# Optimization experiments

Measured on AMD Instinct MI355X. Metric: run time of the kernel, lower is better.

Reference implementation:

```python
import jax
import jax.numpy as jnp
from jax import lax
import numpy as np

DIM = 256
WIN = 7


def setup_inputs() -> dict:
    key = jax.random.key(0)
    ks = jax.random.split(key, 7)
    B, C, H, W = 16, DIM, 64, 64
    k = WIN
    return {
        "x": jax.random.normal(ks[0], (B, C, H, W), dtype=jnp.float32),
        "dw_weight": jax.random.normal(ks[1], (C, 1, k, k), dtype=jnp.float32) * 0.1,
        "pw_weight": jax.random.normal(ks[2], (C, C), dtype=jnp.float32) * 0.05,
        "w1": jax.random.normal(ks[3], (C // 4, C), dtype=jnp.float32) * 0.05,
        "b1": jax.random.normal(ks[4], (C // 4,), dtype=jnp.float32) * 0.05,
        "w2": jax.random.normal(ks[5], (C * k * k, C // 4), dtype=jnp.float32) * 0.05,
        "b2": jax.random.normal(ks[6], (C * k * k,), dtype=jnp.float32) * 0.05,
    }


def reference(x, dw_weight, pw_weight, w1, b1, w2, b2):
    B, C, H, W = x.shape
    k = dw_weight.shape[-1]
    pad = k // 2
    # dynamic kernel generator: global avg pool -> 1x1 conv -> GELU -> 1x1 conv
    pooled = x.mean(axis=(2, 3))                                  # [B, C]
    h = jax.nn.gelu(pooled @ w1.T + b1, approximate=False)        # [B, C//4]
    dyn = (h @ w2.T + b2).reshape(B, C, 1, k, k)                  # [B, C, 1, k, k]
    # fuse static depthwise weights with dynamic per-sample weights
    fused = dw_weight[None] + dyn                                  # [B, C, 1, k, k]
    # per-instance depthwise conv via groups = B*C
    x_flat = x.reshape(1, B * C, H, W)
    kern = fused.reshape(B * C, 1, k, k)
    out = lax.conv_general_dilated(
        x_flat, kern,
        window_strides=(1, 1),
        padding=[(pad, pad), (pad, pad)],
        feature_group_count=B * C,
        dimension_numbers=("NCHW", "OIHW", "NCHW"),
    )
    out = out.reshape(B, C, H, W)
    # final 1x1 pointwise conv (no bias)
    return jnp.einsum("bchw,oc->bohw", out, pw_weight)
```

## Files before the change

kernel.cpp:

```cpp
#include <hip/hip_runtime.h>
#include <math.h>
#include <stdint.h>

typedef __attribute__((ext_vector_type(8))) short short8;
typedef __attribute__((ext_vector_type(4))) float f32x4;

#define B_  16
#define C_  256
#define HW_ 4096
#define KK_ 49
#define CR_ 64

__device__ __forceinline__ ushort f2bf(float f) {
    union { float f; uint32_t u; } v; v.f = f;
    uint32_t r = (v.u + 0x7FFFu + ((v.u >> 16) & 1u)) >> 16;
    return (ushort)r;
}

__global__ __launch_bounds__(256) void pool_kernel(const float* __restrict__ x,
                                                   float* __restrict__ pooled) {
    int bc = blockIdx.x;
    const float4* p4 = (const float4*)(x + (size_t)bc * HW_);
    float s = 0.f;
    for (int i = threadIdx.x; i < HW_ / 4; i += 256) {
        float4 v = p4[i];
        s += (v.x + v.y) + (v.z + v.w);
    }
#pragma unroll
    for (int off = 32; off > 0; off >>= 1) s += __shfl_down(s, off);
    __shared__ float red[4];
    if ((threadIdx.x & 63) == 0) red[threadIdx.x >> 6] = s;
    __syncthreads();
    if (threadIdx.x == 0)
        pooled[bc] = (red[0] + red[1] + red[2] + red[3]) * (1.f / HW_);
}

__global__ __launch_bounds__(64) void mlp_kernel(const float* __restrict__ pooled,
                                                 const float* __restrict__ w1,
                                                 const float* __restrict__ b1,
                                                 float* __restrict__ h) {
    int b = blockIdx.x;
    int r = threadIdx.x;
    __shared__ float pr[C_];
    for (int i = r; i < C_; i += 64) pr[i] = pooled[b * C_ + i];
    __syncthreads();
    float acc = b1[r];
    const float* wr = w1 + (size_t)r * C_;
    for (int c = 0; c < C_; c += 4) {
        float4 wv = *(const float4*)(wr + c);
        acc += pr[c] * wv.x + pr[c + 1] * wv.y + pr[c + 2] * wv.z + pr[c + 3] * wv.w;
    }
    h[b * CR_ + r] = 0.5f * acc * (1.f + erff(acc * 0.70710678118654752f));
}

__global__ __launch_bounds__(256) void genw_kernel(const float* __restrict__ h,
                                                   const float* __restrict__ w2,
                                                   const float* __restrict__ b2,
                                                   const float* __restrict__ dw,
                                                   float* __restrict__ fused) {
    __shared__ float hs[B_ * CR_];
    int m = blockIdx.x * 256 + threadIdx.x;
    for (int i = threadIdx.x; i < B_ * CR_; i += 256) hs[i] = h[i];
    float wrow[CR_];
    const float4* w4 = (const float4*)(w2 + (size_t)m * CR_);
#pragma unroll
    for (int i = 0; i < CR_ / 4; i++) {
        float4 v = w4[i];
        wrow[4 * i] = v.x; wrow[4 * i + 1] = v.y;
        wrow[4 * i + 2] = v.z; wrow[4 * i + 3] = v.w;
    }
    float base = b2[m] + dw[m];
    __syncthreads();
    for (int b = 0; b < B_; b++) {
        float acc = base;
        const float* hb = hs + b * CR_;
#pragma unroll
        for (int r = 0; r < CR_; r++) acc += hb[r] * wrow[r];
        fused[(size_t)b * (C_ * KK_) + m] = acc;
    }
}

__global__ __launch_bounds__(256) void prep_kernel(const float* __restrict__ pw,
                                                   ushort* __restrict__ Pa) {
    int idx = blockIdx.x * 256 + threadIdx.x;
    int o = idx >> 8, c = idx & 255;
    Pa[(size_t)(((o >> 4) * 32) + (c >> 3)) * 128 + (o & 15) * 8 + (c & 7)] = f2bf(pw[idx]);
}

__global__ __launch_bounds__(512, 4) void dw_kernel(const float* __restrict__ x,
                                                    const float* __restrict__ fused,
                                                    ushort* __restrict__ Ug) {
    __shared__ __align__(16) char smem[52352];
    float*  xs  = (float*)smem;
    ushort* Us  = (ushort*)smem;
    float*  wsm = (float*)(smem + 50688);

    const int strip = blockIdx.x;
    const int cb    = blockIdx.y;
    const int b     = blockIdx.z;
    const int tid   = threadIdx.x;
    const int c0    = cb * 8;
    const int r0    = strip * 16;

    for (int i = tid; i < 8 * 22 * 72; i += 512) {
        int ch  = i / 1584;
        int r2  = i - ch * 1584;
        int row = r2 / 72;
        int col = r2 - row * 72;
        int gr = r0 + row - 3, gc = col - 3;
        float v = 0.f;
        if (((unsigned)gr < 64u) && ((unsigned)gc < 64u))
            v = x[(((size_t)b * C_ + c0 + ch) << 12) + (gr << 6) + gc];
        xs[i] = v;
    }
    for (int i = tid; i < 8 * KK_; i += 512) {
        int ch = i / KK_, t = i - ch * KK_;
        wsm[ch * 52 + t] = fused[((size_t)b * C_ + c0 + ch) * KK_ + t];
    }
    __syncthreads();

    const int ch = tid >> 6;
    const int c  = tid & 63;

    float wk[49];
#pragma unroll
    for (int q = 0; q < 12; q++) {
        float4 w4 = *(const float4*)&wsm[ch * 52 + q * 4];
        wk[q * 4 + 0] = w4.x; wk[q * 4 + 1] = w4.y;
        wk[q * 4 + 2] = w4.z; wk[q * 4 + 3] = w4.w;
    }
    wk[48] = wsm[ch * 52 + 48];

    float acc[16];
#pragma unroll
    for (int o = 0; o < 16; o++) acc[o] = 0.f;

    const float* xcol = xs + ch * 1584 + c;
#pragma unroll
    for (int ir = 0; ir < 22; ir++) {
        float x7[7];
#pragma unroll
        for (int j = 0; j < 7; j++) x7[j] = xcol[ir * 72 + j];
        const int olo = (ir - 6 < 0) ? 0 : ir - 6;
        const int ohi = (ir < 15) ? ir : 15;
#pragma unroll
        for (int o = olo; o <= ohi; o++) {
            const int ki = ir - o;
#pragma unroll
            for (int j = 0; j < 7; j++)
                acc[o] = fmaf(x7[j], wk[ki * 7 + j], acc[o]);
        }
    }
    __syncthreads();

#pragma unroll
    for (int o = 0; o < 16; o++)
        Us[(o * 4 + (c >> 4)) * 128 + (c & 15) * 8 + ch] = f2bf(acc[o]);
    __syncthreads();

    for (int t = tid; t < 1024; t += 512) {
        int q = t >> 4, part = t & 15;
        int o = q >> 2, cg = q & 3;
        size_t e = ((((size_t)b * 256) + (size_t)((r0 + o) * 4 + cg)) * 32 + cb) * 128
                   + (size_t)part * 8;
        *(uint4*)(Ug + e) = *(const uint4*)(Us + q * 128 + part * 8);
    }
}

#define GLDS16(gp, lp) __builtin_amdgcn_global_load_lds(\
    (const __attribute__((address_space(1))) uint32_t*)(gp), \
    (__attribute__((address_space(3))) uint32_t*)(lp), 16, 0, 0)

__global__ __launch_bounds__(256, 2) void pw_kernel(const ushort* __restrict__ Pa,
                                                    const ushort* __restrict__ Ug,
                                                    float* __restrict__ Y) {
    __shared__ ushort As[16384];
    __shared__ ushort Bs[8192];
    const int pb   = blockIdx.x;
    const int b    = blockIdx.y;
    const int tid  = threadIdx.x;
    const int w    = tid >> 6;
    const int lane = tid & 63;
    const int oi   = lane & 15;
    const int kq   = lane >> 4;

    f32x4 acc[4][8];
#pragma unroll
    for (int mi = 0; mi < 4; mi++)
#pragma unroll
        for (int ni = 0; ni < 8; ni++)
            acc[mi][ni] = (f32x4){0.f, 0.f, 0.f, 0.f};

    const size_t ubase = (((size_t)b * 256) + (size_t)pb * 8) * 32 * 128;

    for (int kk = 0; kk < 4; kk++) {
        __syncthreads();
        for (int q = w; q < 48; q += 4) {
            const ushort* src; ushort* dst;
            if (q < 32) {
                int obl = q >> 1, half = q & 1;
                src = Pa + (obl * 32 + kk * 8) * 128 + half * 512;
                dst = As + obl * 1024 + half * 512;
            } else {
                int idx = q - 32, pgl = idx >> 1, half = idx & 1;
                src = Ug + ubase + ((size_t)pgl * 32 + kk * 8) * 128 + half * 512;
                dst = Bs + pgl * 1024 + half * 512;
            }
            GLDS16(src + lane * 8, dst);
        }
        asm volatile("s_waitcnt vmcnt(0)" ::: "memory");
        __syncthreads();

        const int abase = w * 4096 + kq * 128 + oi * 8;
        const int bbase = kq * 128 + oi * 8;
#pragma unroll
        for (int ks = 0; ks < 2; ks++) {
            short8 af[4], bf[8];
#pragma unroll
            for (int mi = 0; mi < 4; mi++)
                af[mi] = *(const short8*)&As[abase + mi * 1024 + ks * 512];
#pragma unroll
            for (int ni = 0; ni < 8; ni++)
                bf[ni] = *(const short8*)&Bs[bbase + ni * 1024 + ks * 512];
#pragma unroll
            for (int mi = 0; mi < 4; mi++)
#pragma unroll
                for (int ni = 0; ni < 8; ni++)
                    acc[mi][ni] = __builtin_amdgcn_mfma_f32_16x16x32_bf16(
                        af[mi], bf[ni], acc[mi][ni], 0, 0, 0);
        }
    }
    float* yb = Y + ((size_t)b << 20);
    const int p0 = pb * 128;
#pragma unroll
    for (int mi = 0; mi < 4; mi++) {
#pragma unroll
        for (int ni = 0; ni < 8; ni++) {
            int p = p0 + ni * 16 + oi;
#pragma unroll
            for (int r = 0; r < 4; r++) {
                int o = w * 64 + mi * 16 + kq * 4 + r;
                yb[(size_t)o * HW_ + p] = acc[mi][ni][r];
            }
        }
    }
}

extern "C" void kernel_launch(void* const* d_in, const int* in_sizes, int n_in,
                              void* d_out, int out_size, void* d_ws, size_t ws_size,
                              hipStream_t stream) {
    const float* x  = (const float*)d_in[0];
    const float* dw = (const float*)d_in[1];
    const float* pw = (const float*)d_in[2];
    const float* w1 = (const float*)d_in[3];
    const float* b1 = (const float*)d_in[4];
    const float* w2 = (const float*)d_in[5];
    const float* b2 = (const float*)d_in[6];
    float* out = (float*)d_out;

    char* ws = (char*)d_ws;
    float*  pooled = (float*)(ws);
    float*  h      = (float*)(ws + 16384);
    float*  fused  = (float*)(ws + 20480);
    ushort* Pa     = (ushort*)(ws + 823296);
    ushort* Ug     = (ushort*)(ws + 1048576);

    hipLaunchKernelGGL(pool_kernel, dim3(B_ * C_), dim3(256), 0, stream, x, pooled);
    hipLaunchKernelGGL(mlp_kernel,  dim3(B_), dim3(64), 0, stream, pooled, w1, b1, h);
    hipLaunchKernelGGL(genw_kernel, dim3(49), dim3(256), 0, stream, h, w2, b2, dw, fused);
    hipLaunchKernelGGL(prep_kernel, dim3(256), dim3(256), 0, stream, pw, Pa);
    hipLaunchKernelGGL(dw_kernel,   dim3(4, 32, B_), dim3(512), 0, stream, x, fused, Ug);
    hipLaunchKernelGGL(pw_kernel,   dim3(32, B_), dim3(256), 0, stream, Pa, Ug, out);
}
```

Baseline: 108.0 us.

## Double-buffer pointwise GEMM LDS loads and simplify depthwise tile loading

Result: faster. 100.9 us (-6.5%).

```diff
diff --git a/kernel.cpp b/kernel.cpp
--- a/kernel.cpp
+++ b/kernel.cpp
@@ -90,52 +90,52 @@
 __global__ __launch_bounds__(512, 4) void dw_kernel(const float* __restrict__ x,
                                                     const float* __restrict__ fused,
                                                     ushort* __restrict__ Ug) {
-    __shared__ __align__(16) char smem[52352];
-    float*  xs  = (float*)smem;
-    ushort* Us  = (ushort*)smem;
-    float*  wsm = (float*)(smem + 50688);
+    __shared__ __align__(16) float xs[8 * 22 * 72];
+    ushort* Us = (ushort*)xs;
 
     const int strip = blockIdx.x;
     const int cb    = blockIdx.y;
     const int b     = blockIdx.z;
     const int tid   = threadIdx.x;
+    const int wid   = tid >> 6;
+    const int lane  = tid & 63;
     const int c0    = cb * 8;
     const int r0    = strip * 16;
 
-    for (int i = tid; i < 8 * 22 * 72; i += 512) {
-        int ch  = i / 1584;
-        int r2  = i - ch * 1584;
-        int row = r2 / 72;
-        int col = r2 - row * 72;
-        int gr = r0 + row - 3, gc = col - 3;
-        float v = 0.f;
-        if (((unsigned)gr < 64u) && ((unsigned)gc < 64u))
-            v = x[(((size_t)b * C_ + c0 + ch) << 12) + (gr << 6) + gc];
-        xs[i] = v;
-    }
-    for (int i = tid; i < 8 * KK_; i += 512) {
-        int ch = i / KK_, t = i - ch * KK_;
-        wsm[ch * 52 + t] = fused[((size_t)b * C_ + c0 + ch) * KK_ + t];
-    }
-    __syncthreads();
-
-    const int ch = tid >> 6;
-    const int c  = tid & 63;
+    {
+        const float* xp = x + (((size_t)(b * C_ + c0 + wid)) << 12);
+        float* xd = xs + wid * 1584;
+#pragma unroll
+        for (int row = 0; row < 22; row++) {
+            int gr = r0 + row - 3;
+            float v = 0.f;
+            if ((unsigned)gr < 64u) v = xp[(gr << 6) + lane];
+            xd[row * 72 + 3 + lane] = v;
+        }
+        for (int j = lane; j < 176; j += 64) {
+            int row = j >> 3, e = j & 7;
+            int col = (e < 3) ? e : (64 + e);
+            xd[row * 72 + col] = 0.f;
+        }
+    }
 
     float wk[49];
-#pragma unroll
-    for (int q = 0; q < 12; q++) {
-        float4 w4 = *(const float4*)&wsm[ch * 52 + q * 4];
-        wk[q * 4 + 0] = w4.x; wk[q * 4 + 1] = w4.y;
-        wk[q * 4 + 2] = w4.z; wk[q * 4 + 3] = w4.w;
-    }
-    wk[48] = wsm[ch * 52 + 48];
-
+    {
+        const float* fp = fused + (((size_t)b * C_) + c0 + wid) * KK_;
+        float v = (lane < KK_) ? fp[lane] : 0.f;
+        int vi = __float_as_int(v);
+#pragma unroll
+        for (int t = 0; t < 49; t++)
+            wk[t] = __int_as_float(__builtin_amdgcn_readlane(vi, t));
+    }
+    __syncthreads();
+
+    const int c = lane;
     float acc[16];
 #pragma unroll
     for (int o = 0; o < 16; o++) acc[o] = 0.f;
 
-    const float* xcol = xs + ch * 1584 + c;
+    const float* xcol = xs + wid * 1584 + c;
 #pragma unroll
     for (int ir = 0; ir < 22; ir++) {
         float x7[7];
@@ -155,7 +155,7 @@
 
 #pragma unroll
     for (int o = 0; o < 16; o++)
-        Us[(o * 4 + (c >> 4)) * 128 + (c & 15) * 8 + ch] = f2bf(acc[o]);
+        Us[(o * 4 + (c >> 4)) * 128 + (c & 15) * 8 + wid] = f2bf(acc[o]);
     __syncthreads();
 
     for (int t = tid; t < 1024; t += 512) {
@@ -174,8 +174,8 @@
 __global__ __launch_bounds__(256, 2) void pw_kernel(const ushort* __restrict__ Pa,
                                                     const ushort* __restrict__ Ug,
                                                     float* __restrict__ Y) {
-    __shared__ ushort As[16384];
-    __shared__ ushort Bs[8192];
+    __shared__ ushort As[2][8192];
+    __shared__ ushort Bs[2][4096];
     const int pb   = blockIdx.x;
     const int b    = blockIdx.y;
     const int tid  = threadIdx.x;
@@ -193,43 +193,49 @@
 
     const size_t ubase = (((size_t)b * 256) + (size_t)pb * 8) * 32 * 128;
 
-    for (int kk = 0; kk < 4; kk++) {
-        __syncthreads();
-        for (int q = w; q < 48; q += 4) {
-            const ushort* src; ushort* dst;
-            if (q < 32) {
-                int obl = q >> 1, half = q & 1;
-                src = Pa + (obl * 32 + kk * 8) * 128 + half * 512;
-                dst = As + obl * 1024 + half * 512;
-            } else {
-                int idx = q - 32, pgl = idx >> 1, half = idx & 1;
-                src = Ug + ubase + ((size_t)pgl * 32 + kk * 8) * 128 + half * 512;
-                dst = Bs + pgl * 1024 + half * 512;
-            }
-            GLDS16(src + lane * 8, dst);
-        }
-        asm volatile("s_waitcnt vmcnt(0)" ::: "memory");
-        __syncthreads();
-
-        const int abase = w * 4096 + kq * 128 + oi * 8;
-        const int bbase = kq * 128 + oi * 8;
-#pragma unroll
-        for (int ks = 0; ks < 2; ks++) {
-            short8 af[4], bf[8];
-#pragma unroll
-            for (int mi = 0; mi < 4; mi++)
-                af[mi] = *(const short8*)&As[abase + mi * 1024 + ks * 512];
+#define STAGE(BUF, KB0)                                                          \
+    for (int q = w; q < 24; q += 4) {                                            \
+        const ushort* src; ushort* dst;                                          \
+        if (q < 16) { src = Pa + ((size_t)q * 32 + (KB0)) * 128;                 \
+                      dst = &As[BUF][q * 512]; }                                 \
+        else { int pg = q - 16;                                                  \
+               src = Ug + ubase + ((size_t)pg * 32 + (KB0)) * 128;               \
+               dst = &Bs[BUF][pg * 512]; }                                       \
+        GLDS16(src + lane * 8, dst);                                             \
+    }
+
+    STAGE(0, 0)
+
+#pragma unroll
+    for (int ki = 0; ki < 8; ki++) {
+        const int buf = ki & 1;
+        if (ki < 7) {
+            STAGE(buf ^ 1, (ki + 1) * 4)
+            asm volatile("s_waitcnt vmcnt(6)" ::: "memory");
+        } else {
+            asm volatile("s_waitcnt vmcnt(0)" ::: "memory");
+        }
+        __builtin_amdgcn_s_barrier();
+        __builtin_amdgcn_sched_barrier(0);
+
+        short8 af[4], bf[8];
+#pragma unroll
+        for (int mi = 0; mi < 4; mi++)
+            af[mi] = *(const short8*)&As[buf][(w * 4 + mi) * 512 + kq * 128 + oi * 8];
+#pragma unroll
+        for (int ni = 0; ni < 8; ni++)
+            bf[ni] = *(const short8*)&Bs[buf][ni * 512 + kq * 128 + oi * 8];
+#pragma unroll
+        for (int mi = 0; mi < 4; mi++)
 #pragma unroll
             for (int ni = 0; ni < 8; ni++)
-                bf[ni] = *(const short8*)&Bs[bbase + ni * 1024 + ks * 512];
-#pragma unroll
-            for (int mi = 0; mi < 4; mi++)
-#pragma unroll
-                for (int ni = 0; ni < 8; ni++)
-                    acc[mi][ni] = __builtin_amdgcn_mfma_f32_16x16x32_bf16(
-                        af[mi], bf[ni], acc[mi][ni], 0, 0, 0);
-        }
-    }
+                acc[mi][ni] = __builtin_amdgcn_mfma_f32_16x16x32_bf16(
+                    af[mi], bf[ni], acc[mi][ni], 0, 0, 0);
+
+        __builtin_amdgcn_s_barrier();
+        __builtin_amdgcn_sched_barrier(0);
+    }
+
     float* yb = Y + ((size_t)b << 20);
     const int p0 = pb * 128;
 #pragma unroll
@@ -244,6 +250,7 @@
             }
         }
     }
+#undef STAGE
 }
 
 extern "C" void kernel_launch(void* const* d_in, const int* in_sizes, int n_in,
```
